# Kernel optimization log

Hardware: AMD Instinct MI355X
Metric: run time of the kernel (lower is better)

## Reference

```python
import jax, jax.numpy as jnp
import numpy as np

BETA = 0.9
ADAPT_RATE = 0.1


def _surrogate_spike(x):
    gate = jax.nn.sigmoid(5.0 * x)
    hard = (x > 0).astype(x.dtype)
    return jax.lax.stop_gradient(hard - gate) + gate


def setup_inputs() -> dict:
    key = jax.random.key(0)
    k1, k2, k3, k4, k5 = jax.random.split(key, 5)
    B, T, D, H = 64, 256, 512, 1024
    x = jax.random.normal(k1, (B, T, D), dtype=jnp.float32)
    # fc_in: Linear(D, H); fc_out: Linear(H, 1)
    W_in = jax.random.normal(k2, (H, D), dtype=jnp.float32) * (1.0 / np.sqrt(D))
    b_in = jax.random.normal(k3, (H,), dtype=jnp.float32) * 0.01
    W_out = jax.random.normal(k4, (1, H), dtype=jnp.float32) * (1.0 / np.sqrt(H))
    b_out = jax.random.normal(k5, (1,), dtype=jnp.float32) * 0.01
    return {"x": x, "W_in": W_in, "b_in": b_in, "W_out": W_out, "b_out": b_out}


def reference(x, W_in, b_in, W_out, b_out):
    B, T, D = x.shape
    H = W_in.shape[0]
    # batch fc_in over all timesteps outside the recurrence
    pre = jnp.einsum('btd,hd->bth', x, W_in) + b_in  # [B,T,H]

    def step(carry, p_t):
        mem, adapt = carry
        mem = BETA * mem + p_t - adapt
        spk = _surrogate_spike(mem)
        adapt = adapt + ADAPT_RATE * spk
        mem = mem - spk  # reset_mode == 'subtract'
        return (mem, adapt), spk

    init = (jnp.zeros((B, H), x.dtype), jnp.zeros((B, H), x.dtype))
    _, spks = jax.lax.scan(step, init, jnp.swapaxes(pre, 0, 1))  # spks: [T,B,H]

    # mean_t fc_out(spk_t) == fc_out(mean_t spk_t) since fc_out is affine
    spk_mean = spks.mean(axis=0)  # [B,H]
    return spk_mean @ W_out.T + b_out  # [B,1]
```

## Files before the change

kernel.cpp:

```cpp
#include <hip/hip_runtime.h>

constexpr int Bb = 64;
constexpr int Tt = 256;
constexpr int Dd = 512;
constexpr int Hh = 1024;
constexpr int Mm = Bb * Tt;

typedef _Float16 half8 __attribute__((ext_vector_type(8)));
typedef float floatx16 __attribute__((ext_vector_type(16)));

#define GPTR(x) ((const __attribute__((address_space(1))) void*)(x))
#define LPTR(x) ((__attribute__((address_space(3))) void*)(x))

__global__ __launch_bounds__(256) void convert_t(const float* __restrict__ x,
                                                 const float* __restrict__ Win,
                                                 _Float16* __restrict__ xh,
                                                 _Float16* __restrict__ xl,
                                                 _Float16* __restrict__ wh,
                                                 _Float16* __restrict__ wl,
                                                 const float* __restrict__ bout,
                                                 float* __restrict__ out) {
    const int tid = threadIdx.x;
    if (blockIdx.x == 0 && tid < Bb) out[tid] = bout[0];

    const int gw = (blockIdx.x * 256 + tid) >> 6;
    const int lane = tid & 63;

    const float* src;
    _Float16 *dh, *dl;
    int nrows, kcp, rg;
    if (gw < 8192) {
        src = x; dh = xh; dl = xl; nrows = Mm;
        kcp = gw >> 8;
        rg  = gw & 255;
    } else {
        src = Win; dh = wh; dl = wl; nrows = Hh;
        const int u = gw - 8192;
        kcp = u >> 4;
        rg  = u & 15;
    }
    const int row = rg * 64 + lane;
    const float* p = src + (size_t)row * Dd + kcp * 16;

    const float4 v0 = ((const float4*)p)[0];
    const float4 v1 = ((const float4*)p)[1];
    const float4 v2 = ((const float4*)p)[2];
    const float4 v3 = ((const float4*)p)[3];
    const float va[16] = {v0.x, v0.y, v0.z, v0.w, v1.x, v1.y, v1.z, v1.w,
                          v2.x, v2.y, v2.z, v2.w, v3.x, v3.y, v3.z, v3.w};
    half8 h[2], l[2];
#pragma unroll
    for (int c = 0; c < 2; ++c)
#pragma unroll
        for (int q = 0; q < 8; ++q) {
            const float v = va[c * 8 + q];
            const _Float16 hi = (_Float16)v;
            h[c][q] = hi;
            l[c][q] = (_Float16)((v - (float)hi) * 4096.0f);
        }
#pragma unroll
    for (int c = 0; c < 2; ++c) {
        const size_t g = (size_t)(kcp * 2 + c) * nrows + row;
        *(half8*)(dh + g * 8) = h[c];
        *(half8*)(dl + g * 8) = l[c];
    }
}

__global__ __launch_bounds__(512, 2) void gemm_fused(const _Float16* __restrict__ xh,
                                                     const _Float16* __restrict__ xl,
                                                     const _Float16* __restrict__ wh,
                                                     const _Float16* __restrict__ wl,
                                                     const float* __restrict__ bin,
                                                     const float* __restrict__ Wout,
                                                     float* __restrict__ out) {
    __shared__ _Float16 ldsA[2][2][8192];

    const int tid = threadIdx.x;
    const int id = blockIdx.x;
    const int j  = id & 7;
    const int s  = id >> 3;
    const int nt = s & 7;
    const int b  = (s >> 3) * 8 + j;
    const int m0 = b * Tt;
    const int n0 = nt * 128;

    const int lane = tid & 63;
    const int wave = tid >> 6;
    const int wm = wave & 3;
    const int wn = wave >> 2;
    const int lr = lane & 31;
    const int lk = lane >> 5;

    floatx16 acc[2][2], accx[2][2];
#pragma unroll
    for (int mi = 0; mi < 2; ++mi)
#pragma unroll
        for (int ni = 0; ni < 2; ++ni)
#pragma unroll
            for (int r = 0; r < 16; ++r) { acc[mi][ni][r] = 0.0f; accx[mi][ni][r] = 0.0f; }

#define STAGE_A(buf, kc0)                                                            \
    do {                                                                             \
        _Pragma("unroll")                                                            \
        for (int i_ = 0; i_ < 2; ++i_) {                                             \
            const int c_ = tid + i_ * 512;                                           \
            const int kp_ = c_ >> 8;                                                 \
            const int row_ = c_ & 255;                                               \
            const size_t ga_ = ((size_t)((kc0) + kp_) * Mm + m0 + row_) * 8;         \
            __builtin_amdgcn_global_load_lds(GPTR(xh + ga_), LPTR(&ldsA[buf][0][c_ * 8]), 16, 0, 0); \
            __builtin_amdgcn_global_load_lds(GPTR(xl + ga_), LPTR(&ldsA[buf][1][c_ * 8]), 16, 0, 0); \
        }                                                                            \
    } while (0)

    const size_t bbase = (size_t)(n0 + wn * 64 + lr) * 8;
    half8 bset[2][4];
#define LOAD_B(rot, hs)                                                              \
    do {                                                                             \
        const size_t off_ = (size_t)((hs) * 2 + lk) * (Hh * 8) + bbase;              \
        bset[rot][0] = *(const half8*)(wh + off_);                                   \
        bset[rot][1] = *(const half8*)(wh + off_ + 256);                             \
        bset[rot][2] = *(const half8*)(wl + off_);                                   \
        bset[rot][3] = *(const half8*)(wl + off_ + 256);                             \
    } while (0)

    STAGE_A(0, 0);
    LOAD_B(0, 0);

    for (int ss = 0; ss < 16; ++ss) {
        __syncthreads();
        if (ss < 15) STAGE_A((ss + 1) & 1, (ss + 1) * 4);
        const int cur = ss & 1;
#pragma unroll
        for (int s2 = 0; s2 < 2; ++s2) {
            const int hs = ss * 2 + s2;
            const int rot = hs & 1;
            if (hs < 31) LOAD_B(rot ^ 1, hs + 1);

            half8 ah[2], al[2];
#pragma unroll
            for (int mi = 0; mi < 2; ++mi) {
                const int ci = (s2 * 2 + lk) * 256 + wm * 64 + mi * 32 + lr;
                ah[mi] = *(const half8*)&ldsA[cur][0][ci * 8];
                al[mi] = *(const half8*)&ldsA[cur][1][ci * 8];
            }
#pragma unroll
            for (int mi = 0; mi < 2; ++mi)
#pragma unroll
                for (int ni = 0; ni < 2; ++ni) {
                    acc[mi][ni]  = __builtin_amdgcn_mfma_f32_32x32x16_f16(ah[mi], bset[rot][ni],     acc[mi][ni], 0, 0, 0);
                    accx[mi][ni] = __builtin_amdgcn_mfma_f32_32x32x16_f16(ah[mi], bset[rot][2 + ni], accx[mi][ni], 0, 0, 0);
                    accx[mi][ni] = __builtin_amdgcn_mfma_f32_32x32x16_f16(al[mi], bset[rot][ni],     accx[mi][ni], 0, 0, 0);
                }
        }
    }
#undef STAGE_A
#undef LOAD_B

    float* scanbuf = (float*)ldsA;

    __syncthreads();
#pragma unroll
    for (int p = 0; p < 2; ++p) {
        if (wn == p) {
#pragma unroll
            for (int ni = 0; ni < 2; ++ni) {
                const float bv = bin[n0 + p * 64 + ni * 32 + lr];
#pragma unroll
                for (int mi = 0; mi < 2; ++mi)
#pragma unroll
                    for (int r = 0; r < 16; ++r) {
                        const int row = (r & 3) + 8 * (r >> 2) + 4 * lk;
                        const int t = wm * 64 + mi * 32 + row;
                        scanbuf[ni * 8192 + t * 32 + lr] =
                            acc[mi][ni][r] + accx[mi][ni][r] * (1.0f / 4096.0f) + bv;
                    }
            }
        }
        __syncthreads();
        if (wave == p * 4) {
            const float* sb = scanbuf + (lane >> 5) * 8192 + (lane & 31);
            float mem = 0.0f, adapt = 0.0f, cnt = 0.0f;
#pragma unroll 8
            for (int t = 0; t < Tt; ++t) {
                const float v = sb[t * 32];
                mem = 0.9f * mem + v - adapt;
                const float spk = (mem > 0.0f) ? 1.0f : 0.0f;
                adapt += 0.1f * spk;
                mem -= spk;
                cnt += spk;
            }
            float val = cnt * Wout[n0 + p * 64 + lane] * (1.0f / (float)Tt);
#pragma unroll
            for (int off = 32; off > 0; off >>= 1) val += __shfl_down(val, off, 64);
            if (lane == 0) atomicAdd(&out[b], val);
        }
        if (p == 0) __syncthreads();
    }
}

#define BK 16
#define BMP 132
__global__ __launch_bounds__(256) void gemm_pre(const float* __restrict__ x,
                                                const float* __restrict__ Win,
                                                const float* __restrict__ bin,
                                                float* __restrict__ pre) {
    __shared__ float As[BK][BMP];
    __shared__ float Bs[BK][BMP];
    const int tid = threadIdx.x;
    const int m0 = blockIdx.y * 128;
    const int n0 = blockIdx.x * 128;
    const int tx = tid & 15;
    const int ty = tid >> 4;
    float acc[8][8];
#pragma unroll
    for (int i = 0; i < 8; ++i)
#pragma unroll
        for (int jj = 0; jj < 8; ++jj) acc[i][jj] = 0.0f;
    const float* Aptr = x + (size_t)m0 * Dd;
    const float* Bptr = Win + (size_t)n0 * Dd;
    for (int k0 = 0; k0 < Dd; k0 += BK) {
#pragma unroll
        for (int i = 0; i < 2; ++i) {
            const int lin = tid + i * 256;
            const int row = lin >> 2;
            const int kq = (lin & 3) << 2;
            const float4 av = *(const float4*)(Aptr + (size_t)row * Dd + k0 + kq);
            const float4 bv = *(const float4*)(Bptr + (size_t)row * Dd + k0 + kq);
            As[kq + 0][row] = av.x; As[kq + 1][row] = av.y;
            As[kq + 2][row] = av.z; As[kq + 3][row] = av.w;
            Bs[kq + 0][row] = bv.x; Bs[kq + 1][row] = bv.y;
            Bs[kq + 2][row] = bv.z; Bs[kq + 3][row] = bv.w;
        }
        __syncthreads();
#pragma unroll
        for (int kk = 0; kk < BK; ++kk) {
            const float4 a0 = *(const float4*)&As[kk][ty * 4];
            const float4 a1 = *(const float4*)&As[kk][ty * 4 + 64];
            const float4 b0 = *(const float4*)&Bs[kk][tx * 4];
            const float4 b1 = *(const float4*)&Bs[kk][tx * 4 + 64];
            const float a[8] = {a0.x, a0.y, a0.z, a0.w, a1.x, a1.y, a1.z, a1.w};
            const float b[8] = {b0.x, b0.y, b0.z, b0.w, b1.x, b1.y, b1.z, b1.w};
#pragma unroll
            for (int i = 0; i < 8; ++i)
#pragma unroll
                for (int jj = 0; jj < 8; ++jj) acc[i][jj] += a[i] * b[jj];
        }
        __syncthreads();
    }
#pragma unroll
    for (int i = 0; i < 8; ++i) {
        const int m = m0 + ((i < 4) ? (ty * 4 + i) : (64 + ty * 4 + i - 4));
#pragma unroll
        for (int half = 0; half < 2; ++half) {
            const int n = n0 + tx * 4 + half * 64;
            float4 v;
            v.x = acc[i][half * 4 + 0] + bin[n + 0];
            v.y = acc[i][half * 4 + 1] + bin[n + 1];
            v.z = acc[i][half * 4 + 2] + bin[n + 2];
            v.w = acc[i][half * 4 + 3] + bin[n + 3];
            *(float4*)(pre + (size_t)m * Hh + n) = v;
        }
    }
}

__global__ __launch_bounds__(64) void init_out(const float* __restrict__ bout,
                                               float* __restrict__ out) {
    out[threadIdx.x] = bout[0];
}

__global__ __launch_bounds__(64) void alif_scan(const float* __restrict__ pre,
                                                const float* __restrict__ Wout,
                                                float* __restrict__ out) {
    const int h = blockIdx.x * 64 + threadIdx.x;
    const int b = blockIdx.y;
    const float* p = pre + (size_t)b * Tt * Hh + h;

    float buf[32];
#pragma unroll
    for (int jj = 0; jj < 32; ++jj) buf[jj] = p[(size_t)jj * Hh];

    float mem = 0.0f, adapt = 0.0f, cnt = 0.0f;
    for (int t0 = 0; t0 < Tt; t0 += 32) {
        float cur[32];
#pragma unroll
        for (int jj = 0; jj < 32; ++jj) cur[jj] = buf[jj];
        if (t0 + 32 < Tt) {
#pragma unroll
            for (int jj = 0; jj < 32; ++jj) buf[jj] = p[(size_t)(t0 + 32 + jj) * Hh];
        }
#pragma unroll
        for (int jj = 0; jj < 32; ++jj) {
            mem = 0.9f * mem + cur[jj] - adapt;
            const float spk = (mem > 0.0f) ? 1.0f : 0.0f;
            adapt += 0.1f * spk;
            mem -= spk;
            cnt += spk;
        }
    }

    float val = cnt * Wout[h] * (1.0f / (float)Tt);
#pragma unroll
    for (int off = 32; off > 0; off >>= 1) val += __shfl_down(val, off, 64);
    if (threadIdx.x == 0) atomicAdd(&out[b], val);
}

extern "C" void kernel_launch(void* const* d_in, const int* in_sizes, int n_in,
                              void* d_out, int out_size, void* d_ws, size_t ws_size,
                              hipStream_t stream) {
    const float* x    = (const float*)d_in[0];
    const float* Win  = (const float*)d_in[1];
    const float* bin  = (const float*)d_in[2];
    const float* Wout = (const float*)d_in[3];
    const float* bout = (const float*)d_in[4];
    float* out = (float*)d_out;

    const size_t xh_bytes = (size_t)Mm * Dd * 2;
    const size_t wh_bytes = (size_t)Hh * Dd * 2;
    const size_t need = 2 * xh_bytes + 2 * wh_bytes + 4096;

    if (ws_size >= need) {
        char* base = (char*)d_ws;
        _Float16* xh = (_Float16*)base;
        _Float16* xl = (_Float16*)(base + xh_bytes);
        _Float16* wh = (_Float16*)(base + 2 * xh_bytes);
        _Float16* wl = (_Float16*)(base + 2 * xh_bytes + wh_bytes);

        convert_t<<<2176, 256, 0, stream>>>(x, Win, xh, xl, wh, wl, bout, out);

        gemm_fused<<<512, 512, 0, stream>>>(xh, xl, wh, wl, bin, Wout, out);
    } else {
        float* pre = (float*)d_ws;
        init_out<<<1, 64, 0, stream>>>(bout, out);
        dim3 g1(Hh / 128, Mm / 128);
        gemm_pre<<<g1, 256, 0, stream>>>(x, Win, bin, pre);
        alif_scan<<<dim3(Hh / 64, Bb), 64, 0, stream>>>(pre, Wout, out);
    }
}
```

Before: 159.6 us.

## Fuse x fp16 split conversion into GEMM, stage raw fp32 x via LDS

Stops pre-converting x into hi/lo fp16 arrays in a separate kernel. The GEMM now loads fp32 x directly into LDS and splits it into hi and lo fp16 halves in registers before the MFMAs. Only W_in is still pre-converted. Blocks change from 512 threads covering 128 columns to 256 threads covering 64 columns, with twice as many blocks. This removes a full extra write and read pass over x (32MB fp32 in, 32MB fp16 out), at the cost of redundant conversion ALU work for each N tile and more total blocks that each re-read x.

After: 184.5 us. 15.6% more time.

```diff
diff --git a/kernel.cpp b/kernel.cpp
--- a/kernel.cpp
+++ b/kernel.cpp
@@ -12,10 +12,7 @@
 #define GPTR(x) ((const __attribute__((address_space(1))) void*)(x))
 #define LPTR(x) ((__attribute__((address_space(3))) void*)(x))
 
-__global__ __launch_bounds__(256) void convert_t(const float* __restrict__ x,
-                                                 const float* __restrict__ Win,
-                                                 _Float16* __restrict__ xh,
-                                                 _Float16* __restrict__ xl,
+__global__ __launch_bounds__(256) void convert_w(const float* __restrict__ Win,
                                                  _Float16* __restrict__ wh,
                                                  _Float16* __restrict__ wl,
                                                  const float* __restrict__ bout,
@@ -25,22 +22,10 @@
 
     const int gw = (blockIdx.x * 256 + tid) >> 6;
     const int lane = tid & 63;
-
-    const float* src;
-    _Float16 *dh, *dl;
-    int nrows, kcp, rg;
-    if (gw < 8192) {
-        src = x; dh = xh; dl = xl; nrows = Mm;
-        kcp = gw >> 8;
-        rg  = gw & 255;
-    } else {
-        src = Win; dh = wh; dl = wl; nrows = Hh;
-        const int u = gw - 8192;
-        kcp = u >> 4;
-        rg  = u & 15;
-    }
+    const int kcp = gw >> 4;
+    const int rg  = gw & 15;
     const int row = rg * 64 + lane;
-    const float* p = src + (size_t)row * Dd + kcp * 16;
+    const float* p = Win + (size_t)row * Dd + kcp * 16;
 
     const float4 v0 = ((const float4*)p)[0];
     const float4 v1 = ((const float4*)p)[1];
@@ -60,34 +45,31 @@
         }
 #pragma unroll
     for (int c = 0; c < 2; ++c) {
-        const size_t g = (size_t)(kcp * 2 + c) * nrows + row;
-        *(half8*)(dh + g * 8) = h[c];
-        *(half8*)(dl + g * 8) = l[c];
-    }
-}
-
-__global__ __launch_bounds__(512, 2) void gemm_fused(const _Float16* __restrict__ xh,
-                                                     const _Float16* __restrict__ xl,
+        const size_t g = (size_t)(kcp * 2 + c) * Hh + row;
+        *(half8*)(wh + g * 8) = h[c];
+        *(half8*)(wl + g * 8) = l[c];
+    }
+}
+
+__global__ __launch_bounds__(256, 2) void gemm_fused(const float* __restrict__ x,
                                                      const _Float16* __restrict__ wh,
                                                      const _Float16* __restrict__ wl,
                                                      const float* __restrict__ bin,
                                                      const float* __restrict__ Wout,
                                                      float* __restrict__ out) {
-    __shared__ _Float16 ldsA[2][2][8192];
+    __shared__ float ldsA[2][8192];
 
     const int tid = threadIdx.x;
     const int id = blockIdx.x;
     const int j  = id & 7;
-    const int s  = id >> 3;
-    const int nt = s & 7;
-    const int b  = (s >> 3) * 8 + j;
+    const int q  = id >> 3;
+    const int nt = q & 15;
+    const int b  = (q >> 4) * 8 + j;
     const int m0 = b * Tt;
-    const int n0 = nt * 128;
+    const int n0 = nt * 64;
 
     const int lane = tid & 63;
     const int wave = tid >> 6;
-    const int wm = wave & 3;
-    const int wn = wave >> 2;
     const int lr = lane & 31;
     const int lk = lane >> 5;
 
@@ -99,20 +81,17 @@
 #pragma unroll
             for (int r = 0; r < 16; ++r) { acc[mi][ni][r] = 0.0f; accx[mi][ni][r] = 0.0f; }
 
-#define STAGE_A(buf, kc0)                                                            \
+#define STAGE_A(buf, k0)                                                             \
     do {                                                                             \
         _Pragma("unroll")                                                            \
-        for (int i_ = 0; i_ < 2; ++i_) {                                             \
-            const int c_ = tid + i_ * 512;                                           \
-            const int kp_ = c_ >> 8;                                                 \
-            const int row_ = c_ & 255;                                               \
-            const size_t ga_ = ((size_t)((kc0) + kp_) * Mm + m0 + row_) * 8;         \
-            __builtin_amdgcn_global_load_lds(GPTR(xh + ga_), LPTR(&ldsA[buf][0][c_ * 8]), 16, 0, 0); \
-            __builtin_amdgcn_global_load_lds(GPTR(xl + ga_), LPTR(&ldsA[buf][1][c_ * 8]), 16, 0, 0); \
+        for (int kq_ = 0; kq_ < 8; ++kq_) {                                          \
+            const float* ga_ = x + (size_t)(m0 + tid) * Dd + (k0) + kq_ * 4;         \
+            __builtin_amdgcn_global_load_lds(GPTR(ga_),                              \
+                LPTR(&ldsA[buf][(kq_ * 256 + tid) * 4]), 16, 0, 0);                  \
         }                                                                            \
     } while (0)
 
-    const size_t bbase = (size_t)(n0 + wn * 64 + lr) * 8;
+    const size_t bbase = (size_t)(n0 + lr) * 8;
     half8 bset[2][4];
 #define LOAD_B(rot, hs)                                                              \
     do {                                                                             \
@@ -128,7 +107,7 @@
 
     for (int ss = 0; ss < 16; ++ss) {
         __syncthreads();
-        if (ss < 15) STAGE_A((ss + 1) & 1, (ss + 1) * 4);
+        if (ss < 15) STAGE_A((ss + 1) & 1, (ss + 1) * 32);
         const int cur = ss & 1;
 #pragma unroll
         for (int s2 = 0; s2 < 2; ++s2) {
@@ -139,9 +118,17 @@
             half8 ah[2], al[2];
 #pragma unroll
             for (int mi = 0; mi < 2; ++mi) {
-                const int ci = (s2 * 2 + lk) * 256 + wm * 64 + mi * 32 + lr;
-                ah[mi] = *(const half8*)&ldsA[cur][0][ci * 8];
-                al[mi] = *(const half8*)&ldsA[cur][1][ci * 8];
+                const int fr = wave * 64 + mi * 32 + lr;
+                const int kqb = s2 * 4 + lk * 2;
+                const float4 f0 = *(const float4*)&ldsA[cur][(kqb * 256 + fr) * 4];
+                const float4 f1 = *(const float4*)&ldsA[cur][((kqb + 1) * 256 + fr) * 4];
+                const float fa[8] = {f0.x, f0.y, f0.z, f0.w, f1.x, f1.y, f1.z, f1.w};
+#pragma unroll
+                for (int e = 0; e < 8; ++e) {
+                    const _Float16 hi = (_Float16)fa[e];
+                    ah[mi][e] = hi;
+                    al[mi][e] = (_Float16)((fa[e] - (float)hi) * 4096.0f);
+                }
             }
 #pragma unroll
             for (int mi = 0; mi < 2; ++mi)
@@ -156,45 +143,40 @@
 #undef STAGE_A
 #undef LOAD_B
 
+    __syncthreads();
     float* scanbuf = (float*)ldsA;
 
+#pragma unroll
+    for (int p = 0; p < 2; ++p) {
+        const float bv = bin[n0 + p * 32 + lr];
+#pragma unroll
+        for (int mi = 0; mi < 2; ++mi)
+#pragma unroll
+            for (int r = 0; r < 16; ++r) {
+                const int row = (r & 3) + 8 * (r >> 2) + 4 * lk;
+                const int t = wave * 64 + mi * 32 + row;
+                scanbuf[p * 8192 + t * 32 + lr] =
+                    acc[mi][p][r] + accx[mi][p][r] * (1.0f / 4096.0f) + bv;
+            }
+    }
     __syncthreads();
-#pragma unroll
-    for (int p = 0; p < 2; ++p) {
-        if (wn == p) {
-#pragma unroll
-            for (int ni = 0; ni < 2; ++ni) {
-                const float bv = bin[n0 + p * 64 + ni * 32 + lr];
-#pragma unroll
-                for (int mi = 0; mi < 2; ++mi)
-#pragma unroll
-                    for (int r = 0; r < 16; ++r) {
-                        const int row = (r & 3) + 8 * (r >> 2) + 4 * lk;
-                        const int t = wm * 64 + mi * 32 + row;
-                        scanbuf[ni * 8192 + t * 32 + lr] =
-                            acc[mi][ni][r] + accx[mi][ni][r] * (1.0f / 4096.0f) + bv;
-                    }
-            }
-        }
-        __syncthreads();
-        if (wave == p * 4) {
-            const float* sb = scanbuf + (lane >> 5) * 8192 + (lane & 31);
-            float mem = 0.0f, adapt = 0.0f, cnt = 0.0f;
+
+    if (wave == 0) {
+        const float* sb = scanbuf + (lane >> 5) * 8192 + (lane & 31);
+        float mem = 0.0f, adapt = 0.0f, cnt = 0.0f;
 #pragma unroll 8
-            for (int t = 0; t < Tt; ++t) {
-                const float v = sb[t * 32];
-                mem = 0.9f * mem + v - adapt;
-                const float spk = (mem > 0.0f) ? 1.0f : 0.0f;
-                adapt += 0.1f * spk;
-                mem -= spk;
-                cnt += spk;
-            }
-            float val = cnt * Wout[n0 + p * 64 + lane] * (1.0f / (float)Tt);
-#pragma unroll
-            for (int off = 32; off > 0; off >>= 1) val += __shfl_down(val, off, 64);
-            if (lane == 0) atomicAdd(&out[b], val);
-        }
-        if (p == 0) __syncthreads();
+        for (int t = 0; t < Tt; ++t) {
+            const float v = sb[t * 32];
+            mem = 0.9f * mem + v - adapt;
+            const float spk = (mem > 0.0f) ? 1.0f : 0.0f;
+            adapt += 0.1f * spk;
+            mem -= spk;
+            cnt += spk;
+        }
+        float val = cnt * Wout[n0 + lane] * (1.0f / (float)Tt);
+#pragma unroll
+        for (int off = 32; off > 0; off >>= 1) val += __shfl_down(val, off, 64);
+        if (lane == 0) atomicAdd(&out[b], val);
     }
 }
 
@@ -314,20 +296,15 @@
     const float* bout = (const float*)d_in[4];
     float* out = (float*)d_out;
 
-    const size_t xh_bytes = (size_t)Mm * Dd * 2;
     const size_t wh_bytes = (size_t)Hh * Dd * 2;
-    const size_t need = 2 * xh_bytes + 2 * wh_bytes + 4096;
+    const size_t need = 2 * wh_bytes + 4096;
 
     if (ws_size >= need) {
-        char* base = (char*)d_ws;
-        _Float16* xh = (_Float16*)base;
-        _Float16* xl = (_Float16*)(base + xh_bytes);
-        _Float16* wh = (_Float16*)(base + 2 * xh_bytes);
-        _Float16* wl = (_Float16*)(base + 2 * xh_bytes + wh_bytes);
-
-        convert_t<<<2176, 256, 0, stream>>>(x, Win, xh, xl, wh, wl, bout, out);
-
-        gemm_fused<<<512, 512, 0, stream>>>(xh, xl, wh, wl, bin, Wout, out);
+        _Float16* wh = (_Float16*)d_ws;
+        _Float16* wl = (_Float16*)((char*)d_ws + wh_bytes);
+
+        convert_w<<<128, 256, 0, stream>>>(Win, wh, wl, bout, out);
+        gemm_fused<<<1024, 256, 0, stream>>>(x, wh, wl, bin, Wout, out);
     } else {
         float* pre = (float*)d_ws;
         init_out<<<1, 64, 0, stream>>>(bout, out);
```
